# Optimization experiments

Hardware: AMD Instinct MI355X
Metric: run time of the kernel (lower is better)

Reference implementation:

```python
import jax, jax.numpy as jnp
import numpy as np

B, N, F_IN, F_OUT = 128, 512, 128, 64
ALPHA = 0.2        # LeakyReLU slope for attention logits
GAIN = 1.414       # xavier gain used in the torch module
NEG_INF = -9e15    # mask value from the torch code


def _xavier_uniform(key, shape, gain):
    fan_in, fan_out = shape[0], shape[1]
    limit = gain * np.sqrt(6.0 / (fan_in + fan_out))
    return jax.random.uniform(key, shape, jnp.float32, -limit, limit)


def setup_inputs() -> dict:
    key = jax.random.key(0)
    k1, k2, k3, k4 = jax.random.split(key, 4)
    input_hid = jax.random.normal(k1, (B, N, F_IN), jnp.float32)
    adj = jax.random.randint(k2, (B, N, N), 0, 2, jnp.int32)  # 0/1 adjacency
    W = _xavier_uniform(k3, (F_IN, F_OUT), GAIN)
    a = _xavier_uniform(k4, (2 * F_OUT, 1), GAIN)
    return {"input_hid": input_hid, "adj": adj, "W": W, "a": a}


def reference(input_hid, adj, W, a):
    # h: [B, N, F_OUT]
    h = jnp.matmul(input_hid, W)
    # Standard GAT decomposition of the concat-repeat construction:
    # e[b,i,j] = leakyrelu( [h_i || h_j] @ a ) = leakyrelu( h_i@a_src + h_j@a_dst )
    a_src = a[:F_OUT, 0]   # applies to the repeated-row (i) half
    a_dst = a[F_OUT:, 0]   # applies to the tiled (j) half
    s = jnp.einsum('bnf,f->bn', h, a_src)  # [B, N]
    t = jnp.einsum('bnf,f->bn', h, a_dst)  # [B, N]
    e = jax.nn.leaky_relu(s[:, :, None] + t[:, None, :], ALPHA)  # [B, N, N]
    e = jnp.where(adj > 0, e, NEG_INF)
    att = jax.nn.softmax(e, axis=2)        # softmax over neighbors j
    h_prime = jnp.matmul(att, h)           # [B, N, F_OUT]
    # concat=True -> F.leaky_relu with torch default slope 0.01
    return jax.nn.leaky_relu(h_prime, 0.01)
```

## Files before the change

kernel.cpp:

```cpp
#include <hip/hip_runtime.h>
#include <stdint.h>

#define B_   128
#define N_   512
#define FIN  128
#define FOUT 64

using bf16x8 = __attribute__((ext_vector_type(8))) short;
using f32x4  = __attribute__((ext_vector_type(4))) float;

__device__ inline unsigned short f2bf(float x) {
    union { float f; uint32_t u; } c; c.f = x;
    uint32_t u = c.u;
    return (unsigned short)((u + 0x7FFFu + ((u >> 16) & 1u)) >> 16);
}

__global__ __launch_bounds__(256) void k_h(const float* __restrict__ X,
                                           const float* __restrict__ W,
                                           const float* __restrict__ a,
                                           uint16_t* __restrict__ htT,
                                           float* __restrict__ s,
                                           float* __restrict__ t) {
    __shared__ bf16x8 wl[16 * 64];

    const int b  = blockIdx.x >> 2;
    const int j0 = (blockIdx.x & 3) * 128;
    const int tid = threadIdx.x;
    const int w = tid >> 6, lane = tid & 63;
    const int q = lane >> 4, m = lane & 15;

#pragma unroll
    for (int nt = 0; nt < 4; ++nt) {
        bf16x8 fr;
#pragma unroll
        for (int u = 0; u < 8; ++u)
            fr[u] = (short)f2bf(W[(w * 32 + q * 8 + u) * FOUT + nt * 16 + m]);
        wl[(w * 4 + nt) * 64 + lane] = fr;
    }
    __syncthreads();

    float asv[4], adv[4];
#pragma unroll
    for (int nt = 0; nt < 4; ++nt) {
        asv[nt] = a[nt * 16 + m];
        adv[nt] = a[FOUT + nt * 16 + m];
    }

    const float* xb = X + ((size_t)(b * N_) + j0) * FIN;

    for (int rl = 0; rl < 2; ++rl) {
        const int rt = w + rl * 4;
        const float* xrow = xb + (size_t)(rt * 16 + m) * FIN + q * 8;
        f32x4 acc[4] = {{0.f,0.f,0.f,0.f},{0.f,0.f,0.f,0.f},
                        {0.f,0.f,0.f,0.f},{0.f,0.f,0.f,0.f}};
#pragma unroll
        for (int ks = 0; ks < 4; ++ks) {
            float4 v0 = *(const float4*)(xrow + ks * 32);
            float4 v1 = *(const float4*)(xrow + ks * 32 + 4);
            bf16x8 af;
            af[0] = (short)f2bf(v0.x); af[1] = (short)f2bf(v0.y);
            af[2] = (short)f2bf(v0.z); af[3] = (short)f2bf(v0.w);
            af[4] = (short)f2bf(v1.x); af[5] = (short)f2bf(v1.y);
            af[6] = (short)f2bf(v1.z); af[7] = (short)f2bf(v1.w);
#pragma unroll
            for (int nt = 0; nt < 4; ++nt)
                acc[nt] = __builtin_amdgcn_mfma_f32_16x16x32_bf16(
                    af, wl[(ks * 4 + nt) * 64 + lane], acc[nt], 0, 0, 0);
        }

        float ps[4], pt[4];
#pragma unroll
        for (int r = 0; r < 4; ++r) {
            float vs = 0.f, vt = 0.f;
#pragma unroll
            for (int nt = 0; nt < 4; ++nt) {
                vs += acc[nt][r] * asv[nt];
                vt += acc[nt][r] * adv[nt];
            }
            vs += __shfl_xor(vs, 1, 64); vs += __shfl_xor(vs, 2, 64);
            vs += __shfl_xor(vs, 4, 64); vs += __shfl_xor(vs, 8, 64);
            vt += __shfl_xor(vt, 1, 64); vt += __shfl_xor(vt, 2, 64);
            vt += __shfl_xor(vt, 4, 64); vt += __shfl_xor(vt, 8, 64);
            ps[r] = vs; pt[r] = vt;
        }
        if (m < 4) {
            float vs = (m == 0) ? ps[0] : (m == 1) ? ps[1] : (m == 2) ? ps[2] : ps[3];
            float vt = (m == 0) ? pt[0] : (m == 1) ? pt[1] : (m == 2) ? pt[2] : pt[3];
            int row = j0 + rt * 16 + q * 4 + m;
            s[b * N_ + row] = vs;
            t[b * N_ + row] = vt;
        }

#pragma unroll
        for (int nt = 0; nt < 4; ++nt) {
            uint32_t d0 = (uint32_t)f2bf(acc[nt][0]) | ((uint32_t)f2bf(acc[nt][1]) << 16);
            uint32_t d1 = (uint32_t)f2bf(acc[nt][2]) | ((uint32_t)f2bf(acc[nt][3]) << 16);
            uint2 dd; dd.x = d0; dd.y = d1;
            *(uint2*)(htT + (size_t)(b * FOUT + nt * 16 + m) * N_ + j0 + rt * 16 + q * 4) = dd;
        }
    }
}

__global__ __launch_bounds__(512, 4) void k_attn(const int*    __restrict__ adj,
                                                 const uint16_t* __restrict__ htT,
                                                 const float*  __restrict__ s,
                                                 const float*  __restrict__ t,
                                                 float*        __restrict__ out) {
    __shared__ bf16x8   hstage[64 * 64];
    __shared__ uint32_t lmask[128 * 18];
    __shared__ float    tsh[N_];

    const int bi = blockIdx.x;
    const int b  = bi & 127;
    const int i0 = (bi >> 7) * 128;
    const int tid = threadIdx.x;
    const int w = tid >> 6, lane = tid & 63;
    const int q = lane >> 4, m = lane & 15;

    const uint16_t* hb = htT + (size_t)b * FOUT * N_;

    const int* arow_base = adj + ((size_t)(b * N_) + i0) * N_;
#pragma unroll 2
    for (int r = 0; r < 16; ++r) {
        const int row = w * 16 + r;
        const int* ap = arow_base + (size_t)row * N_;
#pragma unroll
        for (int it = 0; it < 8; ++it) {
            unsigned long long mb = __ballot(ap[it * 64 + lane] > 0);
            if (lane == 0) {
                lmask[row * 18 + it * 2]     = (uint32_t)mb;
                lmask[row * 18 + it * 2 + 1] = (uint32_t)(mb >> 32);
            }
        }
    }

#pragma unroll
    for (int i = 0; i < 8; ++i) {
        int pi = i * 8 + w, ks = pi >> 2, nt = pi & 3;
        hstage[pi * 64 + lane] =
            *(const bf16x8*)(hb + (size_t)(nt * 16 + m) * N_ + ks * 32 + q * 8);
    }
    tsh[tid] = t[b * N_ + tid];
    __syncthreads();

    const int irow = i0 + w * 16 + m;
    const float s_i = s[b * N_ + irow];
    const uint32_t* mymask = &lmask[(w * 16 + m) * 18];

    f32x4 acc[4] = {{0.f,0.f,0.f,0.f},{0.f,0.f,0.f,0.f},
                    {0.f,0.f,0.f,0.f},{0.f,0.f,0.f,0.f}};
    float lsum = 0.f;

#pragma unroll
    for (int ks = 0; ks < 16; ++ks) {
        const uint32_t word = mymask[ks];
        const uint32_t bm = (word >> (q * 8)) & 0xffu;

        const int jb = ks * 32 + q * 8;
        float4 tj0 = *(const float4*)&tsh[jb];
        float4 tj1 = *(const float4*)&tsh[jb + 4];
        float tj[8] = {tj0.x, tj0.y, tj0.z, tj0.w, tj1.x, tj1.y, tj1.z, tj1.w};

        bf16x8 af;
#pragma unroll
        for (int u = 0; u < 8; ++u) {
            float e = s_i + tj[u];
            e = fmaxf(e, 0.2f * e);
            float p = (bm & (1u << u)) ? __expf(e) : 0.0f;
            lsum += p;
            af[u] = (short)f2bf(p);
        }

        bf16x8 bf0 = hstage[(ks * 4 + 0) * 64 + lane];
        bf16x8 bf1 = hstage[(ks * 4 + 1) * 64 + lane];
        bf16x8 bf2 = hstage[(ks * 4 + 2) * 64 + lane];
        bf16x8 bf3 = hstage[(ks * 4 + 3) * 64 + lane];

        acc[0] = __builtin_amdgcn_mfma_f32_16x16x32_bf16(af, bf0, acc[0], 0, 0, 0);
        acc[1] = __builtin_amdgcn_mfma_f32_16x16x32_bf16(af, bf1, acc[1], 0, 0, 0);
        acc[2] = __builtin_amdgcn_mfma_f32_16x16x32_bf16(af, bf2, acc[2], 0, 0, 0);
        acc[3] = __builtin_amdgcn_mfma_f32_16x16x32_bf16(af, bf3, acc[3], 0, 0, 0);
    }

    lsum += __shfl_xor(lsum, 16, 64);
    lsum += __shfl_xor(lsum, 32, 64);

#pragma unroll
    for (int reg = 0; reg < 4; ++reg) {
        float lr = __shfl(lsum, q * 4 + reg, 64);
        float inv = 1.0f / lr;
        int orow = i0 + w * 16 + q * 4 + reg;
        size_t ob = ((size_t)(b * N_) + orow) * FOUT + m;
#pragma unroll
        for (int nt = 0; nt < 4; ++nt) {
            float v = acc[nt][reg] * inv;
            v = fmaxf(v, 0.01f * v);
            out[ob + nt * 16] = v;
        }
    }
}

extern "C" void kernel_launch(void* const* d_in, const int* in_sizes, int n_in,
                              void* d_out, int out_size, void* d_ws, size_t ws_size,
                              hipStream_t stream) {
    const float* X   = (const float*)d_in[0];
    const int*   adj = (const int*)  d_in[1];
    const float* W   = (const float*)d_in[2];
    const float* a   = (const float*)d_in[3];
    float* out = (float*)d_out;

    uint16_t* htT = (uint16_t*)d_ws;
    float* s = (float*)(htT + (size_t)B_ * FOUT * N_);
    float* t = s + B_ * N_;

    k_h<<<B_ * 4, 256, 0, stream>>>(X, W, a, htT, s, t);
    k_attn<<<B_ * 4, 512, 0, stream>>>(adj, htT, s, t, out);
}
```

Before: 282.4 us.

## Move adjacency bitmask packing into a separate high-parallelism kernel

Adds a k_pack kernel that reads the int32 adjacency matrix and writes a packed 1-bit-per-entry mask to workspace, using 16 independent loads per lane before the ballots. k_attn then loads its per-row mask words straight into registers instead of ballot-packing adj into shared memory, which also drops the lmask shared buffer. The goal is to get more memory-level parallelism on the dominant 128 MB adjacency read than the serial ballot loop inside k_attn allowed. In exchange it adds a kernel launch and a small extra mask write and read through global memory.

```diff
diff --git a/kernel.cpp b/kernel.cpp
--- a/kernel.cpp
+++ b/kernel.cpp
@@ -13,6 +13,33 @@
     union { float f; uint32_t u; } c; c.f = x;
     uint32_t u = c.u;
     return (unsigned short)((u + 0x7FFFu + ((u >> 16) & 1u)) >> 16);
+}
+
+__global__ __launch_bounds__(256) void k_pack(const int* __restrict__ adj,
+                                              uint32_t* __restrict__ amask) {
+    const int wid  = (blockIdx.x * 256 + threadIdx.x) >> 6;
+    const int lane = threadIdx.x & 63;
+    const int* base = adj + (size_t)wid * 8192;
+    uint32_t* wout = amask + (size_t)wid * 256;
+
+    for (int it = 0; it < 8; ++it) {
+        const int* p = base + it * 1024;
+        int v[16];
+#pragma unroll
+        for (int s = 0; s < 16; ++s) v[s] = p[s * 64 + lane];
+        unsigned long long bb[16];
+#pragma unroll
+        for (int s = 0; s < 16; ++s) bb[s] = __ballot(v[s] > 0);
+        if (lane == 0) {
+#pragma unroll
+            for (int k = 0; k < 8; ++k) {
+                uint4 d;
+                d.x = (uint32_t)bb[2 * k];     d.y = (uint32_t)(bb[2 * k] >> 32);
+                d.z = (uint32_t)bb[2 * k + 1]; d.w = (uint32_t)(bb[2 * k + 1] >> 32);
+                *(uint4*)(wout + it * 32 + k * 4) = d;
+            }
+        }
+    }
 }
 
 __global__ __launch_bounds__(256) void k_h(const float* __restrict__ X,
@@ -101,14 +128,13 @@
     }
 }
 
-__global__ __launch_bounds__(512, 4) void k_attn(const int*    __restrict__ adj,
+__global__ __launch_bounds__(512, 4) void k_attn(const uint32_t* __restrict__ amask,
                                                  const uint16_t* __restrict__ htT,
                                                  const float*  __restrict__ s,
                                                  const float*  __restrict__ t,
                                                  float*        __restrict__ out) {
-    __shared__ bf16x8   hstage[64 * 64];
-    __shared__ uint32_t lmask[128 * 18];
-    __shared__ float    tsh[N_];
+    __shared__ bf16x8 hstage[64 * 64];
+    __shared__ float  tsh[N_];
 
     const int bi = blockIdx.x;
     const int b  = bi & 127;
@@ -119,20 +145,12 @@
 
     const uint16_t* hb = htT + (size_t)b * FOUT * N_;
 
-    const int* arow_base = adj + ((size_t)(b * N_) + i0) * N_;
-#pragma unroll 2
-    for (int r = 0; r < 16; ++r) {
-        const int row = w * 16 + r;
-        const int* ap = arow_base + (size_t)row * N_;
-#pragma unroll
-        for (int it = 0; it < 8; ++it) {
-            unsigned long long mb = __ballot(ap[it * 64 + lane] > 0);
-            if (lane == 0) {
-                lmask[row * 18 + it * 2]     = (uint32_t)mb;
-                lmask[row * 18 + it * 2 + 1] = (uint32_t)(mb >> 32);
-            }
-        }
-    }
+    const uint32_t* mrow = amask + ((size_t)(b * N_) + i0 + w * 16 + m) * 16;
+    uint32_t mw[16];
+    *(int4*)&mw[0]  = *(const int4*)(mrow);
+    *(int4*)&mw[4]  = *(const int4*)(mrow + 4);
+    *(int4*)&mw[8]  = *(const int4*)(mrow + 8);
+    *(int4*)&mw[12] = *(const int4*)(mrow + 12);
 
 #pragma unroll
     for (int i = 0; i < 8; ++i) {
@@ -143,9 +161,7 @@
     tsh[tid] = t[b * N_ + tid];
     __syncthreads();
 
-    const int irow = i0 + w * 16 + m;
-    const float s_i = s[b * N_ + irow];
-    const uint32_t* mymask = &lmask[(w * 16 + m) * 18];
+    const float s_i = s[b * N_ + i0 + w * 16 + m];
 
     f32x4 acc[4] = {{0.f,0.f,0.f,0.f},{0.f,0.f,0.f,0.f},
                     {0.f,0.f,0.f,0.f},{0.f,0.f,0.f,0.f}};
@@ -153,8 +169,7 @@
 
 #pragma unroll
     for (int ks = 0; ks < 16; ++ks) {
-        const uint32_t word = mymask[ks];
-        const uint32_t bm = (word >> (q * 8)) & 0xffu;
+        const uint32_t bm = (mw[ks] >> (q * 8)) & 0xffu;
 
         const int jb = ks * 32 + q * 8;
         float4 tj0 = *(const float4*)&tsh[jb];
@@ -212,7 +227,9 @@
     uint16_t* htT = (uint16_t*)d_ws;
     float* s = (float*)(htT + (size_t)B_ * FOUT * N_);
     float* t = s + B_ * N_;
-
+    uint32_t* amask = (uint32_t*)(t + B_ * N_);
+
+    k_pack<<<1024, 256, 0, stream>>>(adj, amask);
     k_h<<<B_ * 4, 256, 0, stream>>>(X, W, a, htT, s, t);
-    k_attn<<<B_ * 4, 512, 0, stream>>>(adj, htT, s, t, out);
-}
+    k_attn<<<B_ * 4, 512, 0, stream>>>(amask, htT, s, t, out);
+}
```

Measured after the change: 244.9 us. 1.15x faster.
